# Kernel optimization log

Hardware: AMD Instinct MI355X
Metric: run time of the kernel (lower is better)

Reference implementation:

```python
import jax, jax.numpy as jnp
import numpy as np

# Rows of A/B form separable 3x3 filters via outer product:
#   f0 = identity, f1 = sobel_y, f2 = sobel_x
_A = np.array([[0, 1, 0], [1, 0, -1], [1, 2, 1]], dtype=np.float32)
_B = np.array([[0, 1, 0], [1, 2, 1], [1, 0, -1]], dtype=np.float32)
_LAP = np.array([[0, -1, 0], [-1, 4, -1], [0, -1, 0]], dtype=np.float32)  # 4-connected Laplacian


def _fixed_kernels(C):
    # separable depthwise kernels, torch grouped-conv channel-major order: out idx = c*3 + f
    sep = np.einsum('fi,fj->fij', _A, _B)                       # (3, 3, 3)
    sep_k = np.tile(sep[None], (C, 1, 1, 1)).reshape(C * 3, 1, 3, 3)
    lap_k = np.tile(_LAP[None, None], (C, 1, 1, 1))             # (C, 1, 3, 3)
    return jnp.asarray(sep_k), jnp.asarray(lap_k)


def _conv(xp, k, groups=1):
    # cross-correlation, VALID on already-padded input (matches torch F.conv2d)
    return jax.lax.conv_general_dilated(
        xp, k, window_strides=(1, 1), padding='VALID',
        dimension_numbers=('NCHW', 'OIHW', 'NCHW'),
        feature_group_count=groups)


def setup_inputs() -> dict:
    key = jax.random.key(0)
    k1, k2, k3 = jax.random.split(key, 3)
    N, C, H, W, F = 8, 64, 256, 256, 128
    x = jax.random.normal(k1, (N, C, H, W), dtype=jnp.float32)
    fan_in = C * 9
    W_learned = jax.random.uniform(k2, (F, C, 3, 3), jnp.float32,
                                   -1.0 / np.sqrt(fan_in), 1.0 / np.sqrt(fan_in))
    b_learned = jax.random.uniform(k3, (F,), jnp.float32,
                                   -1.0 / np.sqrt(fan_in), 1.0 / np.sqrt(fan_in))
    return {"x": x, "W_learned": W_learned, "b_learned": b_learned}


def reference(x, W_learned, b_learned):
    C = x.shape[1]
    sep_k, lap_k = _fixed_kernels(C)
    # replicate (edge) pad by 1 on H and W
    xp = jnp.pad(x, ((0, 0), (0, 0), (1, 1), (1, 1)), mode='edge')
    sep = _conv(xp, sep_k, groups=C)                 # (N, 3C, H, W)
    lap = _conv(xp, lap_k, groups=C)                 # (N, C,  H, W)
    learned = _conv(xp, W_learned) + b_learned[None, :, None, None]  # (N, F, H, W)
    return jnp.concatenate([sep, lap, learned], axis=1)
```

## Files before the change

kernel.cpp:

```cpp
#include <hip/hip_runtime.h>

#define HH 256
#define WW 256
#define CC 64
#define FF 128
#define NN 8
#define OUTC 384
#define HW (HH * WW)

typedef __attribute__((ext_vector_type(8))) short bf16x8;
typedef __attribute__((ext_vector_type(4))) float f32x4;

__device__ __forceinline__ int clampi(int v, int lo, int hi) {
    return v < lo ? lo : (v > hi ? hi : v);
}

static __device__ __forceinline__ unsigned short f2bf(float x) {
    unsigned u = __builtin_bit_cast(unsigned, x);
    u += 0x7FFFu + ((u >> 16) & 1u);
    return (unsigned short)(u >> 16);
}
static __device__ __forceinline__ unsigned packbf(float a, float b) {
    return (unsigned)f2bf(a) | ((unsigned)f2bf(b) << 16);
}
static __device__ __forceinline__ float bf2f(unsigned short s) {
    return __builtin_bit_cast(float, (unsigned)s << 16);
}
static __device__ __forceinline__ void nts4(float* p, float a, float b, float c, float d) {
    f32x4 v = {a, b, c, d};
    __builtin_nontemporal_store(v, reinterpret_cast<f32x4*>(p));
}

__global__ __launch_bounds__(256) void wT_kernel(const float* __restrict__ Wl,
                                                 unsigned short* __restrict__ wsW) {
    int e = blockIdx.x * 256 + threadIdx.x;
    if (e >= 9216) return;
    int t = e >> 10;
    int rem = e & 1023;
    int kg = rem >> 7;
    int f = rem & 127;
    unsigned u[4];
#pragma unroll
    for (int j2 = 0; j2 < 4; ++j2) {
        float a = Wl[(size_t)f * 576 + (size_t)(kg * 8 + 2 * j2) * 9 + t];
        float b = Wl[(size_t)f * 576 + (size_t)(kg * 8 + 2 * j2 + 1) * 9 + t];
        u[j2] = packbf(a, b);
    }
    *reinterpret_cast<uint4*>(wsW + (size_t)e * 8) = make_uint4(u[0], u[1], u[2], u[3]);
}

__global__ __launch_bounds__(256) void pack_kernel(const float* __restrict__ x,
                                                   unsigned short* __restrict__ xt) {
    int b = blockIdx.x;
    int y = b & 255;
    int cg = (b >> 8) & 7;
    int n = b >> 11;
    int w = threadIdx.x;
    const float* xp = x + ((size_t)(n * CC + cg * 8)) * HW + (size_t)y * WW + w;
    unsigned u[4];
#pragma unroll
    for (int j2 = 0; j2 < 4; ++j2)
        u[j2] = packbf(xp[(size_t)(2 * j2) * HW], xp[(size_t)(2 * j2 + 1) * HW]);
    *reinterpret_cast<uint4*>(xt + ((size_t)((n * 8 + cg) * HH + y) * WW + w) * 8) =
        make_uint4(u[0], u[1], u[2], u[3]);
}

__global__ __launch_bounds__(256, 4) void mixed_kernel(const unsigned short* __restrict__ wsW,
                                                       const unsigned short* __restrict__ xt,
                                                       const float* __restrict__ bl,
                                                       float* __restrict__ out) {
    __shared__ float lds_e[4][16][68];

    int b = blockIdx.x;
    int g = b / 5;
    int r = b - g * 5;
    int xcd = b & 7;
    int cnt = g >> 3;

    if (r == 0) {
        int n = xcd;
        int y = cnt >> 1;
        int xs = cnt & 1;

        int tid = threadIdx.x;
        int lane = tid & 63;
        int w = tid >> 6;
        int wf = w >> 1;
        int ws = w & 1;
        int x0 = xs * 128 + ws * 64;
        int lr = lane & 15;
        int lk = lane >> 4;

        const char* xb = reinterpret_cast<const char*>(xt) + (size_t)n * (8 * HH * WW * 16);

        int colb[4][3];
#pragma unroll
        for (int j = 0; j < 4; ++j)
#pragma unroll
            for (int dx = 0; dx < 3; ++dx)
                colb[j][dx] = clampi(x0 + j * 16 + lr + dx - 1, 0, WW - 1) * 16;

        f32x4 acc[4][4] = {};

#pragma unroll
        for (int t = 0; t < 9; ++t) {
            int dy = t / 3, dx = t - 3 * (t / 3);
            int yc = clampi(y + dy - 1, 0, HH - 1);
#pragma unroll
            for (int kk = 0; kk < 2; ++kk) {
                int kg = kk * 4 + lk;
                size_t rowoff = ((size_t)kg * HH + yc) * (WW * 16);
                bf16x8 a4[4], b4[4];
#pragma unroll
                for (int mt = 0; mt < 4; ++mt)
                    a4[mt] = *reinterpret_cast<const bf16x8*>(
                        wsW + ((size_t)(t * 8 + kg) * 128 + wf * 64 + mt * 16 + lr) * 8);
#pragma unroll
                for (int j = 0; j < 4; ++j)
                    b4[j] = *reinterpret_cast<const bf16x8*>(xb + rowoff + colb[j][dx]);
#pragma unroll
                for (int mt = 0; mt < 4; ++mt)
#pragma unroll
                    for (int j = 0; j < 4; ++j)
                        acc[mt][j] = __builtin_amdgcn_mfma_f32_16x16x32_bf16(
                            a4[mt], b4[j], acc[mt][j], 0, 0, 0);
            }
        }

        float* le = &lds_e[w][0][0];
#pragma unroll
        for (int mt = 0; mt < 4; ++mt) {
#pragma unroll
            for (int i = 0; i < 4; ++i) {
                int f16 = lk * 4 + i;
                float bv = bl[wf * 64 + mt * 16 + f16];
#pragma unroll
                for (int j = 0; j < 4; ++j)
                    le[f16 * 68 + j * 16 + lr] = acc[mt][j][i] + bv;
            }
#pragma unroll
            for (int p = 0; p < 4; ++p) {
                int f16 = p * 4 + lk;
                const float* s = &le[f16 * 68 + lr * 4];
                int f = wf * 64 + mt * 16 + f16;
                nts4(out + (size_t)(n * OUTC + 256 + f) * HW + (size_t)y * WW + x0 + lr * 4,
                     s[0], s[1], s[2], s[3]);
            }
        }
        return;
    }

    {
        int m = (r - 1) * 512 + cnt;
        int n = xcd;
        int cg = m >> 8;
        int y = m & 255;
        int w = threadIdx.x;

        const unsigned short* xg = xt + (size_t)(n * 8 + cg) * HH * WW * 8;
        int yr[3], wc[3];
#pragma unroll
        for (int d = 0; d < 3; ++d) {
            yr[d] = clampi(y + d - 1, 0, HH - 1);
            wc[d] = clampi(w + d - 1, 0, WW - 1);
        }
        uint4 chunk[3][3];
#pragma unroll
        for (int rr = 0; rr < 3; ++rr)
#pragma unroll
            for (int c = 0; c < 3; ++c)
                chunk[rr][c] = *reinterpret_cast<const uint4*>(
                    xg + ((size_t)yr[rr] * WW + wc[c]) * 8);

        size_t ob = (size_t)n * OUTC * HW + (size_t)y * WW + w;
#pragma unroll
        for (int j = 0; j < 8; ++j) {
            float v[3][3];
#pragma unroll
            for (int rr = 0; rr < 3; ++rr)
#pragma unroll
                for (int c = 0; c < 3; ++c) {
                    unsigned word = (&chunk[rr][c].x)[j >> 1];
                    v[rr][c] = bf2f((unsigned short)(j & 1 ? word >> 16 : word & 0xffff));
                }
            int ch = cg * 8 + j;
            float tL = v[0][0], tC = v[0][1], tR = v[0][2];
            float mL = v[1][0], mC = v[1][1], mR = v[1][2];
            float bL = v[2][0], bC = v[2][1], bR = v[2][2];
            float o0 = mC;
            float o1 = (tL + 2.f * tC + tR) - (bL + 2.f * bC + bR);
            float o2 = (tL - tR) + 2.f * (mL - mR) + (bL - bR);
            float o3 = 4.f * mC - tC - bC - mL - mR;
            __builtin_nontemporal_store(o0, out + ob + (size_t)(ch * 3 + 0) * HW);
            __builtin_nontemporal_store(o1, out + ob + (size_t)(ch * 3 + 1) * HW);
            __builtin_nontemporal_store(o2, out + ob + (size_t)(ch * 3 + 2) * HW);
            __builtin_nontemporal_store(o3, out + ob + (size_t)(192 + ch) * HW);
        }
    }
}

extern "C" void kernel_launch(void* const* d_in, const int* in_sizes, int n_in,
                              void* d_out, int out_size, void* d_ws, size_t ws_size,
                              hipStream_t stream) {
    const float* x  = (const float*)d_in[0];
    const float* Wl = (const float*)d_in[1];
    const float* bl = (const float*)d_in[2];
    float* out = (float*)d_out;

    unsigned short* wsW = (unsigned short*)d_ws;
    unsigned short* xt  = (unsigned short*)((char*)d_ws + 262144);

    wT_kernel<<<36, 256, 0, stream>>>(Wl, wsW);
    pack_kernel<<<16384, 256, 0, stream>>>(x, xt);
    mixed_kernel<<<20480, 256, 0, stream>>>(wsW, xt, bl, out);
}
```

Baseline: 234.2 us.

## Move half of fixed-filter rows into the pack kernel to rebalance work

The pack kernel becomes k1. It now interleaves its packing blocks with blocks that compute the identity, Sobel and Laplacian outputs for rows 0-127 straight from the fp32 input, using float4 row loads. The MFMA kernel (k2) keeps the learned convolution and computes fixed filters only for rows 128-255, so it launches fewer blocks. The aim is to put memory-bound work into the memory-bound pack phase and leave less of it competing with the matrix work in the second kernel. The cost is extra fp32 reads of x for those rows. The two row halves also now compute fixed filters at different precisions (fp32 vs bf16).

```diff
diff --git a/kernel.cpp b/kernel.cpp
--- a/kernel.cpp
+++ b/kernel.cpp
@@ -49,36 +49,86 @@
     *reinterpret_cast<uint4*>(wsW + (size_t)e * 8) = make_uint4(u[0], u[1], u[2], u[3]);
 }
 
-__global__ __launch_bounds__(256) void pack_kernel(const float* __restrict__ x,
-                                                   unsigned short* __restrict__ xt) {
-    int b = blockIdx.x;
-    int y = b & 255;
-    int cg = (b >> 8) & 7;
-    int n = b >> 11;
-    int w = threadIdx.x;
-    const float* xp = x + ((size_t)(n * CC + cg * 8)) * HW + (size_t)y * WW + w;
-    unsigned u[4];
-#pragma unroll
-    for (int j2 = 0; j2 < 4; ++j2)
-        u[j2] = packbf(xp[(size_t)(2 * j2) * HW], xp[(size_t)(2 * j2 + 1) * HW]);
-    *reinterpret_cast<uint4*>(xt + ((size_t)((n * 8 + cg) * HH + y) * WW + w) * 8) =
-        make_uint4(u[0], u[1], u[2], u[3]);
-}
-
-__global__ __launch_bounds__(256, 4) void mixed_kernel(const unsigned short* __restrict__ wsW,
-                                                       const unsigned short* __restrict__ xt,
-                                                       const float* __restrict__ bl,
-                                                       float* __restrict__ out) {
+__global__ __launch_bounds__(256) void k1_kernel(const float* __restrict__ x,
+                                                 unsigned short* __restrict__ xt,
+                                                 float* __restrict__ out) {
+    int bid = blockIdx.x;
+    int xcd = bid & 7;
+    int p = (bid >> 3) & 1;
+    int cnt = bid >> 4;
+    int n = xcd;
+
+    if (p == 0) {
+        int cg = cnt >> 8;
+        int y = cnt & 255;
+        int w = threadIdx.x;
+        const float* xp = x + ((size_t)(n * CC + cg * 8)) * HW + (size_t)y * WW + w;
+        unsigned u[4];
+#pragma unroll
+        for (int j2 = 0; j2 < 4; ++j2)
+            u[j2] = packbf(xp[(size_t)(2 * j2) * HW], xp[(size_t)(2 * j2 + 1) * HW]);
+        *reinterpret_cast<uint4*>(xt + ((size_t)((n * 8 + cg) * HH + y) * WW + w) * 8) =
+            make_uint4(u[0], u[1], u[2], u[3]);
+        return;
+    }
+
+    int c = cnt >> 5;
+    int y4 = cnt & 31;
+    int t = threadIdx.x;
+    int r = t >> 6;
+    int col = (t & 63) * 4;
+    int y = y4 * 4 + r;
+
+    const float* xp = x + ((size_t)(n * CC + c)) * HW;
+    int ym = y == 0 ? 0 : y - 1;
+    int yp = y + 1;
+    int cl = col == 0 ? 0 : col - 1;
+    int cr = (col + 4 > WW - 1) ? WW - 1 : col + 4;
+
+    float4 top = *(const float4*)(xp + (size_t)ym * WW + col);
+    float4 mid = *(const float4*)(xp + (size_t)y  * WW + col);
+    float4 bot = *(const float4*)(xp + (size_t)yp * WW + col);
+    float tl = xp[(size_t)ym * WW + cl], tr = xp[(size_t)ym * WW + cr];
+    float ml = xp[(size_t)y  * WW + cl], mr = xp[(size_t)y  * WW + cr];
+    float blv = xp[(size_t)yp * WW + cl], br = xp[(size_t)yp * WW + cr];
+
+    float tv[6] = {tl, top.x, top.y, top.z, top.w, tr};
+    float mv[6] = {ml, mid.x, mid.y, mid.z, mid.w, mr};
+    float bv[6] = {blv, bot.x, bot.y, bot.z, bot.w, br};
+
+    float o0[4], o1[4], o2[4], o3[4];
+#pragma unroll
+    for (int j = 0; j < 4; ++j) {
+        float tL = tv[j], tC = tv[j + 1], tR = tv[j + 2];
+        float mL = mv[j], mC = mv[j + 1], mR = mv[j + 2];
+        float bL = bv[j], bC = bv[j + 1], bR = bv[j + 2];
+        o0[j] = mC;
+        o1[j] = (tL + 2.0f * tC + tR) - (bL + 2.0f * bC + bR);
+        o2[j] = (tL - tR) + 2.0f * (mL - mR) + (bL - bR);
+        o3[j] = 4.0f * mC - tC - bC - mL - mR;
+    }
+
+    float* ob = out + ((size_t)n * OUTC) * HW + (size_t)y * WW + col;
+    nts4(ob + (size_t)(c * 3 + 0) * HW, o0[0], o0[1], o0[2], o0[3]);
+    nts4(ob + (size_t)(c * 3 + 1) * HW, o1[0], o1[1], o1[2], o1[3]);
+    nts4(ob + (size_t)(c * 3 + 2) * HW, o2[0], o2[1], o2[2], o2[3]);
+    nts4(ob + (size_t)(192 + c)   * HW, o3[0], o3[1], o3[2], o3[3]);
+}
+
+__global__ __launch_bounds__(256, 4) void k2_kernel(const unsigned short* __restrict__ wsW,
+                                                    const unsigned short* __restrict__ xt,
+                                                    const float* __restrict__ bl,
+                                                    float* __restrict__ out) {
     __shared__ float lds_e[4][16][68];
 
-    int b = blockIdx.x;
-    int g = b / 5;
-    int r = b - g * 5;
-    int xcd = b & 7;
-    int cnt = g >> 3;
+    int bid = blockIdx.x;
+    int xcd = bid & 7;
+    int g = bid >> 3;
+    int r = g % 3;
+    int cnt = g / 3;
+    int n = xcd;
 
     if (r == 0) {
-        int n = xcd;
         int y = cnt >> 1;
         int xs = cnt & 1;
 
@@ -152,9 +202,8 @@
 
     {
         int m = (r - 1) * 512 + cnt;
-        int n = xcd;
-        int cg = m >> 8;
-        int y = m & 255;
+        int cg = m >> 7;
+        int y = 128 + (m & 127);
         int w = threadIdx.x;
 
         const unsigned short* xg = xt + (size_t)(n * 8 + cg) * HH * WW * 8;
@@ -211,6 +260,6 @@
     unsigned short* xt  = (unsigned short*)((char*)d_ws + 262144);
 
     wT_kernel<<<36, 256, 0, stream>>>(Wl, wsW);
-    pack_kernel<<<16384, 256, 0, stream>>>(x, xt);
-    mixed_kernel<<<20480, 256, 0, stream>>>(wsW, xt, bl, out);
-}
+    k1_kernel<<<32768, 256, 0, stream>>>(x, xt, out);
+    k2_kernel<<<12288, 256, 0, stream>>>(wsW, xt, bl, out);
+}
```

New measurement: 252.4 us. +7.7%, slower.

## Merge prep kernels and process four rows per depthwise block with rolling window

Applied to the files above, without the earlier changes.

Combines the weight-transpose and input-pack kernels into one launch, saving a kernel launch. The depthwise part now computes four consecutive rows per block and keeps a rolling three-row register window, so each block issues about two new row loads per output row instead of three. The grid is remapped so MFMA and depthwise blocks alternate one-to-one, giving 8192 blocks instead of 20480. In exchange the depthwise blocks do more serial work each and register pressure rises, which may change the balance against the MFMA blocks.

```diff
diff --git a/kernel.cpp b/kernel.cpp
--- a/kernel.cpp
+++ b/kernel.cpp
@@ -31,27 +31,28 @@
     __builtin_nontemporal_store(v, reinterpret_cast<f32x4*>(p));
 }
 
-__global__ __launch_bounds__(256) void wT_kernel(const float* __restrict__ Wl,
-                                                 unsigned short* __restrict__ wsW) {
-    int e = blockIdx.x * 256 + threadIdx.x;
-    if (e >= 9216) return;
-    int t = e >> 10;
-    int rem = e & 1023;
-    int kg = rem >> 7;
-    int f = rem & 127;
-    unsigned u[4];
-#pragma unroll
-    for (int j2 = 0; j2 < 4; ++j2) {
-        float a = Wl[(size_t)f * 576 + (size_t)(kg * 8 + 2 * j2) * 9 + t];
-        float b = Wl[(size_t)f * 576 + (size_t)(kg * 8 + 2 * j2 + 1) * 9 + t];
-        u[j2] = packbf(a, b);
+__global__ __launch_bounds__(256) void prep_kernel(const float* __restrict__ x,
+                                                   const float* __restrict__ Wl,
+                                                   unsigned short* __restrict__ xt,
+                                                   unsigned short* __restrict__ wsW) {
+    int b = blockIdx.x;
+    if (b >= 16384) {
+        int e = (b - 16384) * 256 + threadIdx.x;
+        if (e >= 9216) return;
+        int t = e >> 10;
+        int rem = e & 1023;
+        int kg = rem >> 7;
+        int f = rem & 127;
+        unsigned u[4];
+#pragma unroll
+        for (int j2 = 0; j2 < 4; ++j2) {
+            float a = Wl[(size_t)f * 576 + (size_t)(kg * 8 + 2 * j2) * 9 + t];
+            float bq = Wl[(size_t)f * 576 + (size_t)(kg * 8 + 2 * j2 + 1) * 9 + t];
+            u[j2] = packbf(a, bq);
+        }
+        *reinterpret_cast<uint4*>(wsW + (size_t)e * 8) = make_uint4(u[0], u[1], u[2], u[3]);
+        return;
     }
-    *reinterpret_cast<uint4*>(wsW + (size_t)e * 8) = make_uint4(u[0], u[1], u[2], u[3]);
-}
-
-__global__ __launch_bounds__(256) void pack_kernel(const float* __restrict__ x,
-                                                   unsigned short* __restrict__ xt) {
-    int b = blockIdx.x;
     int y = b & 255;
     int cg = (b >> 8) & 7;
     int n = b >> 11;
@@ -71,14 +72,13 @@
                                                        float* __restrict__ out) {
     __shared__ float lds_e[4][16][68];
 
-    int b = blockIdx.x;
-    int g = b / 5;
-    int r = b - g * 5;
-    int xcd = b & 7;
-    int cnt = g >> 3;
-
-    if (r == 0) {
-        int n = xcd;
+    int bid = blockIdx.x;
+    int xcd = bid & 7;
+    int p = (bid >> 3) & 1;
+    int cnt = bid >> 4;
+    int n = xcd;
+
+    if (p == 0) {
         int y = cnt >> 1;
         int xs = cnt & 1;
 
@@ -139,8 +139,8 @@
                     le[f16 * 68 + j * 16 + lr] = acc[mt][j][i] + bv;
             }
 #pragma unroll
-            for (int p = 0; p < 4; ++p) {
-                int f16 = p * 4 + lk;
+            for (int pp = 0; pp < 4; ++pp) {
+                int f16 = pp * 4 + lk;
                 const float* s = &le[f16 * 68 + lr * 4];
                 int f = wf * 64 + mt * 16 + f16;
                 nts4(out + (size_t)(n * OUTC + 256 + f) * HW + (size_t)y * WW + x0 + lr * 4,
@@ -151,50 +151,59 @@
     }
 
     {
-        int m = (r - 1) * 512 + cnt;
-        int n = xcd;
-        int cg = m >> 8;
-        int y = m & 255;
+        int cg = cnt >> 6;
+        int y0 = (cnt & 63) * 4;
         int w = threadIdx.x;
 
         const unsigned short* xg = xt + (size_t)(n * 8 + cg) * HH * WW * 8;
-        int yr[3], wc[3];
-#pragma unroll
-        for (int d = 0; d < 3; ++d) {
-            yr[d] = clampi(y + d - 1, 0, HH - 1);
-            wc[d] = clampi(w + d - 1, 0, WW - 1);
-        }
-        uint4 chunk[3][3];
-#pragma unroll
-        for (int rr = 0; rr < 3; ++rr)
+        int wc[3];
+#pragma unroll
+        for (int d = 0; d < 3; ++d) wc[d] = clampi(w + d - 1, 0, WW - 1);
+
+        uint4 ch[3][3];
+        int ym = y0 == 0 ? 0 : y0 - 1;
+#pragma unroll
+        for (int c = 0; c < 3; ++c)
+            ch[0][c] = *reinterpret_cast<const uint4*>(xg + ((size_t)ym * WW + wc[c]) * 8);
+#pragma unroll
+        for (int c = 0; c < 3; ++c)
+            ch[1][c] = *reinterpret_cast<const uint4*>(xg + ((size_t)y0 * WW + wc[c]) * 8);
+
+#pragma unroll
+        for (int r = 0; r < 4; ++r) {
+            int yb = y0 + r + 1;
+            if (yb > HH - 1) yb = HH - 1;
 #pragma unroll
             for (int c = 0; c < 3; ++c)
-                chunk[rr][c] = *reinterpret_cast<const uint4*>(
-                    xg + ((size_t)yr[rr] * WW + wc[c]) * 8);
-
-        size_t ob = (size_t)n * OUTC * HW + (size_t)y * WW + w;
-#pragma unroll
-        for (int j = 0; j < 8; ++j) {
-            float v[3][3];
-#pragma unroll
-            for (int rr = 0; rr < 3; ++rr)
+                ch[(r + 2) % 3][c] = *reinterpret_cast<const uint4*>(
+                    xg + ((size_t)yb * WW + wc[c]) * 8);
+
+            const uint4* top = ch[r % 3];
+            const uint4* mid = ch[(r + 1) % 3];
+            const uint4* bot = ch[(r + 2) % 3];
+            size_t ob = (size_t)n * OUTC * HW + (size_t)(y0 + r) * WW + w;
+#pragma unroll
+            for (int j = 0; j < 8; ++j) {
+                float tv[3], mv[3], bv[3];
 #pragma unroll
                 for (int c = 0; c < 3; ++c) {
-                    unsigned word = (&chunk[rr][c].x)[j >> 1];
-                    v[rr][c] = bf2f((unsigned short)(j & 1 ? word >> 16 : word & 0xffff));
+                    unsigned wt = (&top[c].x)[j >> 1];
+                    unsigned wm = (&mid[c].x)[j >> 1];
+                    unsigned wb = (&bot[c].x)[j >> 1];
+                    tv[c] = bf2f((unsigned short)(j & 1 ? wt >> 16 : wt & 0xffff));
+                    mv[c] = bf2f((unsigned short)(j & 1 ? wm >> 16 : wm & 0xffff));
+                    bv[c] = bf2f((unsigned short)(j & 1 ? wb >> 16 : wb & 0xffff));
                 }
-            int ch = cg * 8 + j;
-            float tL = v[0][0], tC = v[0][1], tR = v[0][2];
-            float mL = v[1][0], mC = v[1][1], mR = v[1][2];
-            float bL = v[2][0], bC = v[2][1], bR = v[2][2];
-            float o0 = mC;
-            float o1 = (tL + 2.f * tC + tR) - (bL + 2.f * bC + bR);
-            float o2 = (tL - tR) + 2.f * (mL - mR) + (bL - bR);
-            float o3 = 4.f * mC - tC - bC - mL - mR;
-            __builtin_nontemporal_store(o0, out + ob + (size_t)(ch * 3 + 0) * HW);
-            __builtin_nontemporal_store(o1, out + ob + (size_t)(ch * 3 + 1) * HW);
-            __builtin_nontemporal_store(o2, out + ob + (size_t)(ch * 3 + 2) * HW);
-            __builtin_nontemporal_store(o3, out + ob + (size_t)(192 + ch) * HW);
+                int chn = cg * 8 + j;
+                float o0 = mv[1];
+                float o1 = (tv[0] + 2.f * tv[1] + tv[2]) - (bv[0] + 2.f * bv[1] + bv[2]);
+                float o2 = (tv[0] - tv[2]) + 2.f * (mv[0] - mv[2]) + (bv[0] - bv[2]);
+                float o3 = 4.f * mv[1] - tv[1] - bv[1] - mv[0] - mv[2];
+                __builtin_nontemporal_store(o0, out + ob + (size_t)(chn * 3 + 0) * HW);
+                __builtin_nontemporal_store(o1, out + ob + (size_t)(chn * 3 + 1) * HW);
+                __builtin_nontemporal_store(o2, out + ob + (size_t)(chn * 3 + 2) * HW);
+                __builtin_nontemporal_store(o3, out + ob + (size_t)(192 + chn) * HW);
+            }
         }
     }
 }
@@ -210,7 +219,6 @@
     unsigned short* wsW = (unsigned short*)d_ws;
     unsigned short* xt  = (unsigned short*)((char*)d_ws + 262144);
 
-    wT_kernel<<<36, 256, 0, stream>>>(Wl, wsW);
-    pack_kernel<<<16384, 256, 0, stream>>>(x, xt);
-    mixed_kernel<<<20480, 256, 0, stream>>>(wsW, xt, bl, out);
-}
+    prep_kernel<<<16420, 256, 0, stream>>>(x, Wl, xt, wsW);
+    mixed_kernel<<<8192, 256, 0, stream>>>(wsW, xt, bl, out);
+}
```

Result: slower. 286.1 us (+22.1%).
